# Kernel tuning notes

Measured on AMD Instinct MI355X. Metric: run time of the kernel, lower is better.

## Reference

```python
import jax, jax.numpy as jnp
import numpy as np

# Module constants (from source defaults)
KERNEL_SIZES = (2, 3, 4, 5)
KERNEL_NUMS = (2, 3, 4, 5)  # sum = 14 -> fc in_features
EMB_DIM = 100
NUM_CLASSES = 5
VOCAB = 100000
B, L = 512, 512


def setup_inputs() -> dict:
    key = jax.random.key(0)
    ks = jax.random.split(key, 12)
    words = jax.random.randint(ks[0], (B, L), 0, VOCAB)
    # Dense w2v table replacing the per-token vocab/gensim lookup (OOV rows would be zeros;
    # a random dense table is equivalent math for the gather).
    emb_table = jax.random.normal(ks[1], (VOCAB, EMB_DIM), dtype=jnp.float32) * 0.1
    inp = {"words": words, "emb_table": emb_table}
    for i, (ksz, knum) in enumerate(zip(KERNEL_SIZES, KERNEL_NUMS)):
        inp[f"w{ksz}"] = jax.random.normal(ks[2 + i], (knum, EMB_DIM, ksz), dtype=jnp.float32) * 0.05
        inp[f"b{ksz}"] = jnp.zeros((knum,), dtype=jnp.float32)
    inp["fc_w"] = jax.random.normal(ks[10], (NUM_CLASSES, sum(KERNEL_NUMS)), dtype=jnp.float32) * 0.1
    inp["fc_b"] = jnp.zeros((NUM_CLASSES,), dtype=jnp.float32)
    return inp


def _conv_relu_maxpool(x, w, b):
    # x: [B, D, L], w: [O, D, k] -> conv1d VALID, relu, max over time -> [B, O]
    y = jax.lax.conv_general_dilated(
        x, w, window_strides=(1,), padding="VALID",
        dimension_numbers=("NCH", "OIH", "NCH"))
    y = jax.nn.relu(y + b[None, :, None])
    return jnp.max(y, axis=-1)


def reference(words, emb_table, w2, b2, w3, b3, w4, b4, w5, b5, fc_w, fc_b):
    # Embedding gather (replaces the serial per-token Python loop)
    x = emb_table[words]                 # [B, L, D]
    x = jnp.transpose(x, (0, 2, 1))      # [B, D, L]
    feats = jnp.concatenate([
        _conv_relu_maxpool(x, w2, b2),
        _conv_relu_maxpool(x, w3, b3),
        _conv_relu_maxpool(x, w4, b4),
        _conv_relu_maxpool(x, w5, b5),
    ], axis=1)                           # [B, 14]
    # dropout is identity at inference
    return feats @ fc_w.T + fc_b         # [B, NUM_CLASSES]
```

## Files before the change

### kernel.cpp

```cpp
#include <hip/hip_runtime.h>
#include <hip/hip_bf16.h>

#define BATCH 512
#define SEQL  512
#define VOCAB 100000
#define NCH   14
#define NCLS  5


#define WSB_OFF     0
#define BIAS_OFF    16384
#define CONTRIB_OFF 32768

typedef __attribute__((ext_vector_type(8))) short bf16x8;
typedef __attribute__((ext_vector_type(4))) float f32x4;

static __device__ __forceinline__ unsigned short bf16bits(float f) {
    __hip_bfloat16 h = __float2bfloat16(f);
    return __builtin_bit_cast(unsigned short, h);
}
static __device__ __forceinline__ float bf16f(unsigned int hbits) {
    union { unsigned int u; float f; } x; x.u = hbits << 16; return x.f;
}
static __device__ __forceinline__ unsigned int getdw(const uint4& u, int w) {
    switch (w) { case 0: return u.x; case 1: return u.y; case 2: return u.z; default: return u.w; }
}

__global__ void repack_w(
    const float* __restrict__ w2, const float* __restrict__ b2,
    const float* __restrict__ w3, const float* __restrict__ b3,
    const float* __restrict__ w4, const float* __restrict__ b4,
    const float* __restrict__ w5, const float* __restrict__ b5,
    unsigned short* __restrict__ wsb, float* __restrict__ biasf)
{
    const float* WP[4] = {w2, w3, w4, w5};
    const int gi = blockIdx.x * 256 + threadIdx.x;
    if (gi < 8192) {
        int nt = gi >> 11;
        int ks = (gi >> 9) & 3;
        int l  = (gi >> 3) & 63;
        int e  = gi & 7;
        int n  = nt * 16 + (l & 15);
        int k  = ks * 32 + ((l >> 4) << 3) + e;
        int j = -1, c = 0;
        if (n < 14)                 { j = 0; c = n; }
        else if (n >= 16 && n < 30) { j = 1; c = n - 16; }
        else if (n >= 32 && n < 44) { j = 2; c = 2 + (n - 32); }
        else if (n >= 44 && n < 53) { j = 3; c = 5 + (n - 44); }
        else if (n >= 53 && n < 58) { j = 4; c = 9 + (n - 53); }
        float v = 0.f;
        if (j >= 0 && k < 100) {
            int kc  = 2 + (c >= 2) + (c >= 5) + (c >= 9);
            int grp = (c >= 2) + (c >= 5) + (c >= 9);
            int ob  = (grp == 0) ? 0 : (grp == 1) ? 2 : (grp == 2) ? 5 : 9;
            v = WP[grp][((c - ob) * 100 + k) * kc + j];
        }
        wsb[gi] = bf16bits(v);
    }
    if (blockIdx.x == 0 && threadIdx.x < 16) {
        const int t = threadIdx.x;
        float bv = 0.f;
        if (t < 2)        bv = b2[t];
        else if (t < 5)   bv = b3[t - 2];
        else if (t < 9)   bv = b4[t - 5];
        else if (t < NCH) bv = b5[t - 9];
        biasf[t] = bv;
    }
}

__global__ __launch_bounds__(256, 4) void contrib_gemm(
    const float* __restrict__ emb,
    const char* __restrict__ ws,
    unsigned short* __restrict__ contrib)
{
    __shared__ unsigned short xs[64 * 128];
    const int v0  = blockIdx.x * 64;
    const int tid = threadIdx.x;
    const int l   = tid & 63;
    const int wt  = tid >> 6;

    const float4* __restrict__ emb4 = reinterpret_cast<const float4*>(emb);
    uint2* xs2 = reinterpret_cast<uint2*>(xs);
    #pragma unroll
    for (int it = 0; it < 8; ++it) {
        const int i = tid + it * 256;
        const int r = i >> 5;
        const int q = i & 31;
        const int v = v0 + r;
        uint lo = 0, hi = 0;
        if (v < VOCAB && q < 25) {
            float4 x = emb4[(long)v * 25 + q];
            lo = (uint)bf16bits(x.x) | ((uint)bf16bits(x.y) << 16);
            hi = (uint)bf16bits(x.z) | ((uint)bf16bits(x.w) << 16);
        }
        const int addr = (r * 256 + q * 8) ^ ((r & 7) << 4);
        xs2[addr >> 3] = make_uint2(lo, hi);
    }
    __syncthreads();

    f32x4 acc[4] = {{0.f,0.f,0.f,0.f},{0.f,0.f,0.f,0.f},
                    {0.f,0.f,0.f,0.f},{0.f,0.f,0.f,0.f}};
    const char* xsb = reinterpret_cast<const char*>(xs);
    const int arow = wt * 16 + (l & 15);
    const int dl   = (l >> 4) << 3;
    #pragma unroll
    for (int ks = 0; ks < 4; ++ks) {
        const int aad = (arow * 256 + (ks * 32 + dl) * 2) ^ ((arow & 7) << 4);
        bf16x8 a = *reinterpret_cast<const bf16x8*>(xsb + aad);
        #pragma unroll
        for (int nt = 0; nt < 4; ++nt) {
            bf16x8 bf = *reinterpret_cast<const bf16x8*>(
                ws + WSB_OFF + ((nt * 4 + ks) * 64 + l) * 16);
            acc[nt] = __builtin_amdgcn_mfma_f32_16x16x32_bf16(a, bf, acc[nt], 0, 0, 0);
        }
    }

    const int vbase = v0 + wt * 16 + ((l >> 4) << 2);
    #pragma unroll
    for (int nt = 0; nt < 4; ++nt) {
        #pragma unroll
        for (int r = 0; r < 4; ++r) {
            const int v = vbase + r;
            if (v < VOCAB)
                contrib[(long)v * 64 + nt * 16 + (l & 15)] = bf16bits(acc[nt][r]);
        }
    }
}

__global__ __launch_bounds__(512, 4) void gather_max_fc(
    const int* __restrict__ words,
    const unsigned short* __restrict__ contrib,
    const float* __restrict__ biasf,
    const float* __restrict__ fcw, const float* __restrict__ fcb,
    float* __restrict__ out)
{
    __shared__ float red[8][NCH];
    __shared__ float sfin[NCH];

    const int b  = blockIdx.x;
    const int t  = threadIdx.x;
    const int l  = t & 63;
    const int wv = t >> 6;

    constexpr int KC[NCH]  = {2,2, 3,3,3, 4,4,4,4, 5,5,5,5,5};
    constexpr int SIDX[5]  = {0,16,32,44,53};
    constexpr int CST[5]   = {0,0,2,5,9};
    constexpr int B0[5]    = {0,2,4,5,6};

    int tok[5];
    #pragma unroll
    for (int j = 0; j < 5; ++j) {
        int u = t + j; if (u > SEQL - 1) u = SEQL - 1;
        tok[j] = words[b * SEQL + u];
    }

    uint4 u0[5], u1[5];
    #pragma unroll
    for (int j = 0; j < 5; ++j) {
        const uint4* rp = reinterpret_cast<const uint4*>(contrib + (long)tok[j] * 64);
        u0[j] = rp[B0[j]];
        u1[j] = rp[B0[j] + 1];
    }

    float y[NCH];
    #pragma unroll
    for (int c = 0; c < NCH; ++c) {
        float s = 0.f;
        #pragma unroll
        for (int j = 0; j < 5; ++j) {
            if (j < KC[c]) {
                const int n   = SIDX[j] + (c - CST[j]);
                const int rel = 2 * n - 16 * B0[j];
                const int w   = rel >> 2;
                const int h   = (rel >> 1) & 1;
                const unsigned int dw = (w < 4) ? getdw(u0[j], w) : getdw(u1[j], w - 4);
                s += bf16f(h ? (dw >> 16) : (dw & 0xffffu));
            }
        }
        y[c] = s;
    }

    #pragma unroll
    for (int c = 0; c < NCH; ++c) {
        float v = 0.f;
        if (t + KC[c] <= SEQL) v = fmaxf(y[c] + biasf[c], 0.f);
        #pragma unroll
        for (int off = 32; off > 0; off >>= 1)
            v = fmaxf(v, __shfl_xor(v, off, 64));
        if (l == 0) red[wv][c] = v;
    }
    __syncthreads();
    if (t < NCH) {
        float f = red[0][t];
        #pragma unroll
        for (int w = 1; w < 8; ++w) f = fmaxf(f, red[w][t]);
        sfin[t] = f;
    }
    __syncthreads();
    if (t < NCLS) {
        float acc = fcb[t];
        #pragma unroll
        for (int o = 0; o < NCH; ++o) acc += fcw[t * NCH + o] * sfin[o];
        out[b * NCLS + t] = acc;
    }
}

extern "C" void kernel_launch(void* const* d_in, const int* in_sizes, int n_in,
                              void* d_out, int out_size, void* d_ws, size_t ws_size,
                              hipStream_t stream) {
    const int*   words = (const int*)  d_in[0];
    const float* emb   = (const float*)d_in[1];
    const float* w2    = (const float*)d_in[2];
    const float* b2    = (const float*)d_in[3];
    const float* w3    = (const float*)d_in[4];
    const float* b3    = (const float*)d_in[5];
    const float* w4    = (const float*)d_in[6];
    const float* b4    = (const float*)d_in[7];
    const float* w5    = (const float*)d_in[8];
    const float* b5    = (const float*)d_in[9];
    const float* fcw   = (const float*)d_in[10];
    const float* fcb   = (const float*)d_in[11];
    float* out = (float*)d_out;
    char*  ws  = (char*)d_ws;

    unsigned short* wsb     = (unsigned short*)(ws + WSB_OFF);
    float*          biasf   = (float*)(ws + BIAS_OFF);
    unsigned short* contrib = (unsigned short*)(ws + CONTRIB_OFF);

    hipLaunchKernelGGL(repack_w, dim3(32), dim3(256), 0, stream,
                       w2, b2, w3, b3, w4, b4, w5, b5, wsb, biasf);
    hipLaunchKernelGGL(contrib_gemm, dim3((VOCAB + 63) / 64), dim3(256), 0, stream,
                       emb, ws, contrib);
    hipLaunchKernelGGL(gather_max_fc, dim3(BATCH), dim3(512), 0, stream,
                       words, contrib, biasf, fcw, fcb, out);
}
```

Measured before the change: 34.84 us.

## Make contrib GEMM persistent with double-buffered LDS and register-resident weights

The contrib GEMM becomes a persistent grid of 521 blocks, each handling three 64-row vocab tiles. The B-fragments are loaded once into registers, and the next tile's embedding loads are issued before the MFMAs on the current tile so they overlap through a double-buffered LDS. Embedding reads and contrib writes use nontemporal hints. The goal is to hide global-load latency and avoid reloading weights per tile, at the cost of more registers and fewer resident blocks per CU.

```diff
diff --git a/kernel.cpp b/kernel.cpp
--- a/kernel.cpp
+++ b/kernel.cpp
@@ -6,6 +6,7 @@
 #define VOCAB 100000
 #define NCH   14
 #define NCLS  5
+#define GBLK  521
 
 
 #define WSB_OFF     0
@@ -14,6 +15,7 @@
 
 typedef __attribute__((ext_vector_type(8))) short bf16x8;
 typedef __attribute__((ext_vector_type(4))) float f32x4;
+typedef __attribute__((ext_vector_type(4))) float fvec4;
 
 static __device__ __forceinline__ unsigned short bf16bits(float f) {
     __hip_bfloat16 h = __float2bfloat16(f);
@@ -68,62 +70,91 @@
     }
 }
 
-__global__ __launch_bounds__(256, 4) void contrib_gemm(
+__global__ __launch_bounds__(256, 2) void contrib_gemm(
     const float* __restrict__ emb,
     const char* __restrict__ ws,
     unsigned short* __restrict__ contrib)
 {
-    __shared__ unsigned short xs[64 * 128];
-    const int v0  = blockIdx.x * 64;
+    __shared__ unsigned short xs[2][64 * 128];
+    const int bid = blockIdx.x;
     const int tid = threadIdx.x;
     const int l   = tid & 63;
     const int wt  = tid >> 6;
 
-    const float4* __restrict__ emb4 = reinterpret_cast<const float4*>(emb);
-    uint2* xs2 = reinterpret_cast<uint2*>(xs);
-    #pragma unroll
-    for (int it = 0; it < 8; ++it) {
-        const int i = tid + it * 256;
-        const int r = i >> 5;
-        const int q = i & 31;
-        const int v = v0 + r;
-        uint lo = 0, hi = 0;
-        if (v < VOCAB && q < 25) {
-            float4 x = emb4[(long)v * 25 + q];
-            lo = (uint)bf16bits(x.x) | ((uint)bf16bits(x.y) << 16);
-            hi = (uint)bf16bits(x.z) | ((uint)bf16bits(x.w) << 16);
-        }
-        const int addr = (r * 256 + q * 8) ^ ((r & 7) << 4);
-        xs2[addr >> 3] = make_uint2(lo, hi);
-    }
-    __syncthreads();
-
-    f32x4 acc[4] = {{0.f,0.f,0.f,0.f},{0.f,0.f,0.f,0.f},
-                    {0.f,0.f,0.f,0.f},{0.f,0.f,0.f,0.f}};
-    const char* xsb = reinterpret_cast<const char*>(xs);
+    bf16x8 bfrag[16];
+    #pragma unroll
+    for (int f = 0; f < 16; ++f)
+        bfrag[f] = *reinterpret_cast<const bf16x8*>(ws + WSB_OFF + (f * 64 + l) * 16);
+
+    const fvec4* __restrict__ emb4 = reinterpret_cast<const fvec4*>(emb);
+
+    auto stage_load = [&](int tile, fvec4 (&pre)[8]) {
+        const int v0 = tile * 64;
+        #pragma unroll
+        for (int it = 0; it < 8; ++it) {
+            const int i = tid + it * 256;
+            const int r = i >> 5;
+            const int q = i & 31;
+            const int v = v0 + r;
+            if (v < VOCAB && q < 25)
+                pre[it] = __builtin_nontemporal_load(emb4 + (long)v * 25 + q);
+            else
+                pre[it] = (fvec4){0.f, 0.f, 0.f, 0.f};
+        }
+    };
+    auto stage_write = [&](int buf, const fvec4 (&pre)[8]) {
+        uint2* xs2 = reinterpret_cast<uint2*>(xs[buf]);
+        #pragma unroll
+        for (int it = 0; it < 8; ++it) {
+            const int i = tid + it * 256;
+            const int r = i >> 5;
+            const int q = i & 31;
+            const uint lo = (uint)bf16bits(pre[it][0]) | ((uint)bf16bits(pre[it][1]) << 16);
+            const uint hi = (uint)bf16bits(pre[it][2]) | ((uint)bf16bits(pre[it][3]) << 16);
+            const int addr = (r * 256 + q * 8) ^ ((r & 7) << 4);
+            xs2[addr >> 3] = make_uint2(lo, hi);
+        }
+    };
+
+    fvec4 pre[8];
+    stage_load(bid, pre);
+    stage_write(0, pre);
+
     const int arow = wt * 16 + (l & 15);
     const int dl   = (l >> 4) << 3;
-    #pragma unroll
-    for (int ks = 0; ks < 4; ++ks) {
-        const int aad = (arow * 256 + (ks * 32 + dl) * 2) ^ ((arow & 7) << 4);
-        bf16x8 a = *reinterpret_cast<const bf16x8*>(xsb + aad);
+
+    #pragma unroll 1
+    for (int s = 0; s < 3; ++s) {
+        __syncthreads();
+        if (s < 2) stage_load(bid + (s + 1) * GBLK, pre);
+
+        f32x4 acc[4] = {{0.f,0.f,0.f,0.f},{0.f,0.f,0.f,0.f},
+                        {0.f,0.f,0.f,0.f},{0.f,0.f,0.f,0.f}};
+        const char* xsb = reinterpret_cast<const char*>(xs[s & 1]);
+        #pragma unroll
+        for (int ks = 0; ks < 4; ++ks) {
+            const int aad = (arow * 256 + (ks * 32 + dl) * 2) ^ ((arow & 7) << 4);
+            bf16x8 a = *reinterpret_cast<const bf16x8*>(xsb + aad);
+            #pragma unroll
+            for (int nt = 0; nt < 4; ++nt)
+                acc[nt] = __builtin_amdgcn_mfma_f32_16x16x32_bf16(
+                    a, bfrag[nt * 4 + ks], acc[nt], 0, 0, 0);
+        }
+
+        const int tile  = bid + s * GBLK;
+        const int vbase = tile * 64 + wt * 16 + ((l >> 4) << 2);
         #pragma unroll
         for (int nt = 0; nt < 4; ++nt) {
-            bf16x8 bf = *reinterpret_cast<const bf16x8*>(
-                ws + WSB_OFF + ((nt * 4 + ks) * 64 + l) * 16);
-            acc[nt] = __builtin_amdgcn_mfma_f32_16x16x32_bf16(a, bf, acc[nt], 0, 0, 0);
-        }
-    }
-
-    const int vbase = v0 + wt * 16 + ((l >> 4) << 2);
-    #pragma unroll
-    for (int nt = 0; nt < 4; ++nt) {
-        #pragma unroll
-        for (int r = 0; r < 4; ++r) {
-            const int v = vbase + r;
-            if (v < VOCAB)
-                contrib[(long)v * 64 + nt * 16 + (l & 15)] = bf16bits(acc[nt][r]);
-        }
+            #pragma unroll
+            for (int r = 0; r < 4; ++r) {
+                const int v = vbase + r;
+                if (v < VOCAB)
+                    __builtin_nontemporal_store(bf16bits(acc[nt][r]),
+                        &contrib[(long)v * 64 + nt * 16 + (l & 15)]);
+            }
+        }
+
+        if (s < 2) stage_write((s & 1) ^ 1, pre);
     }
 }
 
@@ -229,7 +260,7 @@
 
     hipLaunchKernelGGL(repack_w, dim3(32), dim3(256), 0, stream,
                        w2, b2, w3, b3, w4, b4, w5, b5, wsb, biasf);
-    hipLaunchKernelGGL(contrib_gemm, dim3((VOCAB + 63) / 64), dim3(256), 0, stream,
+    hipLaunchKernelGGL(contrib_gemm, dim3(GBLK), dim3(256), 0, stream,
                        emb, ws, contrib);
     hipLaunchKernelGGL(gather_max_fc, dim3(BATCH), dim3(512), 0, stream,
                        words, contrib, biasf, fcw, fcb, out);
```

Result: slower. 40.90 us (+17.4%).
